# Optimization experiments

Hardware: AMD Instinct MI355X
Metric: run time of the kernel (lower is better)

The kernel has to match this reference:

```python
import jax, jax.numpy as jnp
import numpy as np

S, B, D, H = 2048, 2, 2048, 16
HD = D // H  # 128
EPS = 1e-5


def _layernorm(x, w, b):
    mu = jnp.mean(x, axis=-1, keepdims=True)
    var = jnp.mean((x - mu) ** 2, axis=-1, keepdims=True)
    return (x - mu) * jax.lax.rsqrt(var + EPS) * w + b


def _apply_rotary(x, freqs_cis):
    # x: [B, S, H, HD]; freqs_cis: [S, HD//2, 2]
    xr = x.astype(jnp.float32).reshape(x.shape[0], x.shape[1], x.shape[2], HD // 2, 2)
    f = freqs_cis.reshape(1, xr.shape[1], 1, xr.shape[3], 2)
    out = jnp.stack(
        [xr[..., 0] * f[..., 0] - xr[..., 1] * f[..., 1],
         xr[..., 1] * f[..., 0] + xr[..., 0] * f[..., 1]],
        axis=-1,
    )
    return out.reshape(x.shape).astype(x.dtype)


def setup_inputs() -> dict:
    key = jax.random.key(0)
    ks = jax.random.split(key, 6)
    scale = 0.02
    return {
        "x": jax.random.normal(ks[0], (S, B, D), dtype=jnp.float32),
        "freqs_cis": jax.random.normal(ks[1], (S, HD // 2, 2), dtype=jnp.float32),
        "wqkv_w": jax.random.normal(ks[2], (3 * D, D), dtype=jnp.float32) * scale,
        "wqkv_b": jnp.zeros((3 * D,), dtype=jnp.float32),
        "wo_w": jax.random.normal(ks[3], (D, D), dtype=jnp.float32) * scale,
        "wo_b": jnp.zeros((D,), dtype=jnp.float32),
        "qn_w": jnp.ones((HD,), dtype=jnp.float32),
        "qn_b": jnp.zeros((HD,), dtype=jnp.float32),
        "kn_w": jnp.ones((HD,), dtype=jnp.float32),
        "kn_b": jnp.zeros((HD,), dtype=jnp.float32),
    }


def reference(x, freqs_cis, wqkv_w, wqkv_b, wo_w, wo_b, qn_w, qn_b, kn_w, kn_b):
    # x: [S, B, D] -> [B, S, D]
    xb = jnp.transpose(x, (1, 0, 2))
    qkv = jnp.einsum("bsd,ed->bse", xb, wqkv_w) + wqkv_b  # [B, S, 3D]
    xq, xk, xv = jnp.split(qkv, 3, axis=-1)
    xq = xq.reshape(B, S, H, HD)
    xk = xk.reshape(B, S, H, HD)
    xv = xv.reshape(B, S, H, HD)
    # QK-norm over head_dim
    xq = _layernorm(xq, qn_w, qn_b)
    xk = _layernorm(xk, kn_w, kn_b)
    # RoPE
    xq = _apply_rotary(xq, freqs_cis)
    xk = _apply_rotary(xk, freqs_cis)
    # [B, H, S, HD]
    q = jnp.transpose(xq, (0, 2, 1, 3))
    k = jnp.transpose(xk, (0, 2, 1, 3))
    v = jnp.transpose(xv, (0, 2, 1, 3))
    scores = jnp.einsum("bhqd,bhkd->bhqk", q, k) / jnp.sqrt(jnp.float32(HD))
    causal = jnp.tril(jnp.ones((S, S), dtype=bool))
    scores = jnp.where(causal, scores, jnp.finfo(scores.dtype).min)
    attn = jax.nn.softmax(scores, axis=-1)
    out = jnp.einsum("bhqk,bhkd->bhqd", attn, v)  # [B, H, S, HD]
    out = jnp.transpose(out, (0, 2, 1, 3)).reshape(B, S, D)
    out = jnp.einsum("bsd,ed->bse", out, wo_w) + wo_b
    return jnp.transpose(out, (1, 0, 2))  # [S, B, D]
```

## Files before the change

### kernel.cpp

```cpp
#include <hip/hip_runtime.h>
#include <hip/hip_bf16.h>

#define S 2048
#define B 2
#define D 2048
#define H 16
#define HD 128
#define N3 6144
#define KD 2048

typedef __hip_bfloat16 bf16;
typedef float f32x4 __attribute__((ext_vector_type(4)));
typedef short short8 __attribute__((ext_vector_type(8)));
typedef short sv4 __attribute__((ext_vector_type(4)));

__device__ __forceinline__ void gload16(const void* g, void* l) {
    __builtin_amdgcn_global_load_lds((const __attribute__((address_space(1))) void*)g,
                                     (__attribute__((address_space(3))) void*)l, 16, 0, 0);
}
__device__ __forceinline__ void bar() {
    asm volatile("" ::: "memory");
    __builtin_amdgcn_s_barrier();
    asm volatile("" ::: "memory");
}

__global__ __launch_bounds__(256) void cvt_x_kernel(const float* __restrict__ x, bf16* __restrict__ xb) {
    int i = blockIdx.x * 256 + threadIdx.x;
    int d  = i & (D - 1);
    int sb = i >> 11;
    int b  = sb & (B - 1);
    int s  = sb >> 1;
    xb[((size_t)(b * S + s) << 11) + d] = __float2bfloat16(x[i]);
}

__global__ __launch_bounds__(256) void cvt_w_kernel(const float* __restrict__ in, bf16* __restrict__ o, int n) {
    for (int i = blockIdx.x * blockDim.x + threadIdx.x; i < n; i += gridDim.x * blockDim.x)
        o[i] = __float2bfloat16(in[i]);
}

template <int MODE>
__global__ __launch_bounds__(256, 2) void gemm128(
    const bf16* __restrict__ A, const bf16* __restrict__ W, const float* __restrict__ bias,
    bf16* __restrict__ oq, bf16* __restrict__ ok, bf16* __restrict__ ovT,
    float* __restrict__ oOut)
{
    constexpr int NT = KD / 64;

    __shared__ __align__(16) bf16 SA[2][128 * 64];
    __shared__ __align__(16) bf16 SB[2][128 * 64];

    const int tid = threadIdx.x;
    const int w = tid >> 6, l = tid & 63;
    const int wm = w >> 1, wn = w & 1;
    const int l15 = l & 15, l4 = l >> 4;

    const int id  = blockIdx.y * gridDim.x + blockIdx.x;
    const int xcd = id & 7;
    const int j   = id >> 3;
    const int npx = gridDim.x >> 3;
    const int tileN = (xcd * npx + j % npx) * 128;
    const int tileM = (j / npx) * 128;

    const int lrow8 = l >> 3;
    const int lsb   = ((l & 7) * 16) ^ (lrow8 << 4);
    const int rxor  = (l15 & 7) << 3;

    const char* AgT = (const char*)A + (size_t)tileM * (KD * 2);
    const char* WgT = (const char*)W + (size_t)tileN * (KD * 2);

    auto stage_tile = [&](int buf, int kt) {
#pragma unroll
        for (int j2 = 0; j2 < 4; ++j2) {
            const int chunk = w * 4 + j2;
            gload16(AgT + (size_t)(chunk * 8 + lrow8) * (KD * 2) + kt * 128 + lsb,
                    (char*)&SA[buf][0] + chunk * 1024);
        }
#pragma unroll
        for (int j2 = 0; j2 < 4; ++j2) {
            const int chunk = w * 4 + j2;
            gload16(WgT + (size_t)(chunk * 8 + lrow8) * (KD * 2) + kt * 128 + lsb,
                    (char*)&SB[buf][0] + chunk * 1024);
        }
    };

    f32x4 acc[4][4] = {};

#define TILE_BODY(BUF, KTN)                                                                \
    {                                                                                      \
        stage_tile(BUF ^ 1, KTN);                                                          \
        _Pragma("unroll") for (int kk = 0; kk < 2; ++kk) {                                 \
            short8 bfrag[4], afr[4];                                                       \
            _Pragma("unroll") for (int ni = 0; ni < 4; ++ni)                               \
                bfrag[ni] = *(const short8*)&SB[BUF][(wn * 64 + ni * 16 + l15) * 64 +      \
                                                     ((kk * 32 + l4 * 8) ^ rxor)];         \
            _Pragma("unroll") for (int q = 0; q < 4; ++q)                                  \
                afr[q] = *(const short8*)&SA[BUF][(wm * 64 + q * 16 + l15) * 64 +          \
                                                  ((kk * 32 + l4 * 8) ^ rxor)];            \
            __builtin_amdgcn_s_setprio(1);                                                 \
            _Pragma("unroll") for (int q = 0; q < 4; ++q)                                  \
                _Pragma("unroll") for (int ni = 0; ni < 4; ++ni)                           \
                    acc[q][ni] = __builtin_amdgcn_mfma_f32_16x16x32_bf16(                  \
                        afr[q], bfrag[ni], acc[q][ni], 0, 0, 0);                           \
            __builtin_amdgcn_s_setprio(0);                                                 \
        }                                                                                  \
        asm volatile("s_waitcnt vmcnt(0)" ::: "memory");                                   \
        bar();                                                                             \
    }

    stage_tile(0, 0);
    asm volatile("s_waitcnt vmcnt(0)" ::: "memory");
    bar();

#pragma unroll 1
    for (int t = 0; t < NT; t += 2) {
        const int tn1 = (t + 1 < NT) ? t + 1 : NT - 1;
        const int tn2 = (t + 2 < NT) ? t + 2 : NT - 1;
        TILE_BODY(0, tn1)
        TILE_BODY(1, tn2)
    }
#undef TILE_BODY

#pragma unroll
    for (int mi = 0; mi < 4; ++mi) {
#pragma unroll
        for (int ni = 0; ni < 4; ++ni) {
            const int ncol = tileN + wn * 64 + ni * 16 + l15;
            const float bv = bias[ncol];
            const int m0 = tileM + wm * 64 + mi * 16 + l4 * 4;
            if (MODE == 0) {
                const int b_ = m0 >> 11, s0 = m0 & (S - 1);
                const int which = ncol >> 11;
                const int hh = (ncol >> 7) & (H - 1);
                const int hd = ncol & (HD - 1);
                const int bh = b_ * H + hh;
                if (which == 2) {
                    sv4 pk;
#pragma unroll
                    for (int r = 0; r < 4; ++r) {
                        __hip_bfloat16 t = __float2bfloat16(acc[mi][ni][r] + bv);
                        pk[r] = reinterpret_cast<short&>(t);
                    }
                    *(sv4*)&ovT[((size_t)bh * HD + hd) * S + s0] = pk;
                } else {
                    bf16* dst = which ? ok : oq;
#pragma unroll
                    for (int r = 0; r < 4; ++r)
                        dst[((size_t)bh * S + s0 + r) * HD + hd] =
                            __float2bfloat16(acc[mi][ni][r] + bv);
                }
            } else {
#pragma unroll
                for (int r = 0; r < 4; ++r) {
                    const int m = m0 + r;
                    const int b_ = m >> 11, s_ = m & (S - 1);
                    oOut[((size_t)s_ * B + b_) * D + ncol] = acc[mi][ni][r] + bv;
                }
            }
        }
    }
}

__global__ __launch_bounds__(256) void ln_rope_kernel(
    bf16* __restrict__ q, bf16* __restrict__ k,
    const float* __restrict__ fc,
    const float* __restrict__ qw, const float* __restrict__ qb,
    const float* __restrict__ kw, const float* __restrict__ kb)
{
    const int tid = threadIdx.x;
    const int w = tid >> 6, l = tid & 63;
    const int row = blockIdx.x * 4 + w;
    const int s_ = row & (S - 1);
    const size_t base = (size_t)row * HD;
    const float f0 = fc[s_ * HD + 2 * l];
    const float f1 = fc[s_ * HD + 2 * l + 1];

#pragma unroll
    for (int which = 0; which < 2; ++which) {
        bf16* p = which == 0 ? q : k;
        const float* gw = which == 0 ? qw : kw;
        const float* gb = which == 0 ? qb : kb;
        const float osc = which == 0 ? 0.08838834764831845f : 1.0f;
        float x0 = __bfloat162float(p[base + 2 * l]);
        float x1 = __bfloat162float(p[base + 2 * l + 1]);
        float sm = x0 + x1;
#pragma unroll
        for (int msk = 1; msk < 64; msk <<= 1) sm += __shfl_xor(sm, msk);
        const float mu = sm * (1.0f / HD);
        const float d0 = x0 - mu, d1 = x1 - mu;
        float vs = d0 * d0 + d1 * d1;
#pragma unroll
        for (int msk = 1; msk < 64; msk <<= 1) vs += __shfl_xor(vs, msk);
        const float rstd = rsqrtf(vs * (1.0f / HD) + 1e-5f);
        const float n0 = d0 * rstd * gw[2 * l] + gb[2 * l];
        const float n1 = d1 * rstd * gw[2 * l + 1] + gb[2 * l + 1];
        p[base + 2 * l]     = __float2bfloat16((n0 * f0 - n1 * f1) * osc);
        p[base + 2 * l + 1] = __float2bfloat16((n1 * f0 + n0 * f1) * osc);
    }
}

__global__ __launch_bounds__(256, 2) void attn_kernel(
    const bf16* __restrict__ q, const bf16* __restrict__ k, const bf16* __restrict__ vT,
    bf16* __restrict__ out)
{
    __shared__ __align__(16) bf16 KT[2][64 * 128];
    __shared__ __align__(16) bf16 VS[2][128 * 64];
    __shared__ __align__(16) bf16 Pb[4][16 * 72];

    const int tid = threadIdx.x, w = tid >> 6, l = tid & 63;
    const int l15 = l & 15, l4 = l >> 4;

    const int id  = blockIdx.y * gridDim.x + blockIdx.x;
    const int nid = (id & 7) * 64 + (id >> 3);
    const int bh  = nid >> 4;
    const int pr  = nid & 15;
    const int qtA = 31 - pr;
    const int qtB = pr;

    const int b_ = bh >> 4, hh = bh & (H - 1);
    const int qrA = qtA * 64 + w * 16;
    const int qrB = qtB * 64 + w * 16;
    const size_t hQ = (size_t)bh * S * HD;
    const size_t hV = (size_t)bh * HD * S;

    const char* kbase = (const char*)(k + hQ);
    const char* vbase = (const char*)(vT + hV);
    int ksrc[4], vsrc[4], kdst[4], vdst[4];
#pragma unroll
    for (int j = 0; j < 4; ++j) {
        const int ik = w * 4 + j;
        const int rt = ik * 4 + (l >> 4);
        ksrc[j] = rt * 256 + (((l & 15) * 16) ^ ((rt & 15) << 4));
        kdst[j] = ik * 1024;
        const int rd = ik * 8 + (l >> 3);
        vsrc[j] = rd * (S * 2) + (((l & 7) * 16) ^ ((rd & 7) << 4));
        vdst[j] = ik * 1024;
    }

    short8 aqA[4], aqB[4];
#pragma unroll
    for (int c = 0; c < 4; ++c) {
        aqA[c] = *(const short8*)&q[hQ + (size_t)(qrA + l15) * HD + c * 32 + l4 * 8];
        aqB[c] = *(const short8*)&q[hQ + (size_t)(qrB + l15) * HD + c * 32 + l4 * 8];
    }

    f32x4 oA[8] = {}, oB[8] = {};
    float psA[4] = {0.f, 0.f, 0.f, 0.f}, psB[4] = {0.f, 0.f, 0.f, 0.f};

#pragma unroll
    for (int j = 0; j < 4; ++j)
        gload16(kbase + ksrc[j], (char*)KT[0] + kdst[j]);

    const int kx = l15 << 3;
    const int vx = (l15 & 7) << 3;
    const float LOG2E = 1.4426950408889634f;
    const float SHIFT = -23.083120654223414f;

    for (int kvt = 0; kvt <= qtA; ++kvt) {
        const int kvb = kvt * 64;
        const int cur = kvt & 1;
        const bool doB = (kvt <= qtB);
#pragma unroll
        for (int j = 0; j < 4; ++j)
            gload16(vbase + (size_t)kvb * 2 + vsrc[j], (char*)VS[cur] + vdst[j]);
        if (kvt < qtA) {
#pragma unroll
            for (int j = 0; j < 4; ++j)
                gload16(kbase + (size_t)(kvb + 64) * 256 + ksrc[j], (char*)KT[cur ^ 1] + kdst[j]);
        }
        if (kvt < qtA) { asm volatile("s_waitcnt vmcnt(8)" ::: "memory"); }
        else           { asm volatile("s_waitcnt vmcnt(4)" ::: "memory"); }
        bar();

        short8 apA[2], apB[2];
        {
            f32x4 sacc[4] = {};
#pragma unroll
            for (int c = 0; c < 4; ++c) {
                const int cole = (c * 32 + l4 * 8) ^ kx;
#pragma unroll
                for (int n = 0; n < 4; ++n) {
                    short8 bk = *(const short8*)&KT[cur][(n * 16 + l15) * 128 + cole];
                    sacc[n] = __builtin_amdgcn_mfma_f32_16x16x32_bf16(aqA[c], bk, sacc[n], 0, 0, 0);
                }
            }
            if (kvt == qtA) {
#pragma unroll
                for (int n = 0; n < 4; ++n)
#pragma unroll
                    for (int r = 0; r < 4; ++r) {
                        float sv = (kvb + n * 16 + l15 > qrA + l4 * 4 + r) ? -1e30f : sacc[n][r];
                        const float pv = __builtin_amdgcn_exp2f(__builtin_fmaf(sv, LOG2E, SHIFT));
                        sacc[n][r] = pv; psA[r] += pv;
                    }
            } else {
#pragma unroll
                for (int n = 0; n < 4; ++n)
#pragma unroll
                    for (int r = 0; r < 4; ++r) {
                        const float pv = __builtin_amdgcn_exp2f(__builtin_fmaf(sacc[n][r], LOG2E, SHIFT));
                        sacc[n][r] = pv; psA[r] += pv;
                    }
            }
#pragma unroll
            for (int n = 0; n < 4; ++n)
#pragma unroll
                for (int r = 0; r < 4; ++r)
                    Pb[w][(l4 * 4 + r) * 72 + n * 16 + l15] = __float2bfloat16(sacc[n][r]);
#pragma unroll
            for (int c = 0; c < 2; ++c)
                apA[c] = *(const short8*)&Pb[w][l15 * 72 + c * 32 + l4 * 8];
        }
        if (doB) {
            f32x4 sacc[4] = {};
#pragma unroll
            for (int c = 0; c < 4; ++c) {
                const int cole = (c * 32 + l4 * 8) ^ kx;
#pragma unroll
                for (int n = 0; n < 4; ++n) {
                    short8 bk = *(const short8*)&KT[cur][(n * 16 + l15) * 128 + cole];
                    sacc[n] = __builtin_amdgcn_mfma_f32_16x16x32_bf16(aqB[c], bk, sacc[n], 0, 0, 0);
                }
            }
            if (kvt == qtB) {
#pragma unroll
                for (int n = 0; n < 4; ++n)
#pragma unroll
                    for (int r = 0; r < 4; ++r) {
                        float sv = (kvb + n * 16 + l15 > qrB + l4 * 4 + r) ? -1e30f : sacc[n][r];
                        const float pv = __builtin_amdgcn_exp2f(__builtin_fmaf(sv, LOG2E, SHIFT));
                        sacc[n][r] = pv; psB[r] += pv;
                    }
            } else {
#pragma unroll
                for (int n = 0; n < 4; ++n)
#pragma unroll
                    for (int r = 0; r < 4; ++r) {
                        const float pv = __builtin_amdgcn_exp2f(__builtin_fmaf(sacc[n][r], LOG2E, SHIFT));
                        sacc[n][r] = pv; psB[r] += pv;
                    }
            }
#pragma unroll
            for (int n = 0; n < 4; ++n)
#pragma unroll
                for (int r = 0; r < 4; ++r)
                    Pb[w][(l4 * 4 + r) * 72 + n * 16 + l15] = __float2bfloat16(sacc[n][r]);
#pragma unroll
            for (int c = 0; c < 2; ++c)
                apB[c] = *(const short8*)&Pb[w][l15 * 72 + c * 32 + l4 * 8];
        }

        if (kvt < qtA) { asm volatile("s_waitcnt vmcnt(4)" ::: "memory"); }
        else           { asm volatile("s_waitcnt vmcnt(0)" ::: "memory"); }
        bar();

#pragma unroll
        for (int c = 0; c < 2; ++c) {
#pragma unroll
            for (int d = 0; d < 8; ++d) {
                const int rd = d * 16 + l15;
                short8 bv = *(const short8*)&VS[cur][rd * 64 + ((c * 32 + l4 * 8) ^ vx)];
                oA[d] = __builtin_amdgcn_mfma_f32_16x16x32_bf16(apA[c], bv, oA[d], 0, 0, 0);
            }
        }
        if (doB) {
#pragma unroll
            for (int c = 0; c < 2; ++c) {
#pragma unroll
                for (int d = 0; d < 8; ++d) {
                    const int rd = d * 16 + l15;
                    short8 bv = *(const short8*)&VS[cur][rd * 64 + ((c * 32 + l4 * 8) ^ vx)];
                    oB[d] = __builtin_amdgcn_mfma_f32_16x16x32_bf16(apB[c], bv, oB[d], 0, 0, 0);
                }
            }
        }
    }

#pragma unroll
    for (int r = 0; r < 4; ++r) {
#pragma unroll
        for (int msk = 1; msk < 16; msk <<= 1) psA[r] += __shfl_xor(psA[r], msk);
        const float inv = 1.0f / psA[r];
        const int s_ = qrA + l4 * 4 + r;
        const size_t obase = ((size_t)b_ * S + s_) * D + hh * HD;
#pragma unroll
        for (int d = 0; d < 8; ++d)
            out[obase + d * 16 + l15] = __float2bfloat16(oA[d][r] * inv);
    }
#pragma unroll
    for (int r = 0; r < 4; ++r) {
#pragma unroll
        for (int msk = 1; msk < 16; msk <<= 1) psB[r] += __shfl_xor(psB[r], msk);
        const float inv = 1.0f / psB[r];
        const int s_ = qrB + l4 * 4 + r;
        const size_t obase = ((size_t)b_ * S + s_) * D + hh * HD;
#pragma unroll
        for (int d = 0; d < 8; ++d)
            out[obase + d * 16 + l15] = __float2bfloat16(oB[d][r] * inv);
    }
}

extern "C" void kernel_launch(void* const* d_in, const int* in_sizes, int n_in,
                              void* d_out, int out_size, void* d_ws, size_t ws_size,
                              hipStream_t stream) {
    const float* x      = (const float*)d_in[0];
    const float* fc     = (const float*)d_in[1];
    const float* wqkv_w = (const float*)d_in[2];
    const float* wqkv_b = (const float*)d_in[3];
    const float* wo_w   = (const float*)d_in[4];
    const float* wo_b   = (const float*)d_in[5];
    const float* qn_w   = (const float*)d_in[6];
    const float* qn_b   = (const float*)d_in[7];
    const float* kn_w   = (const float*)d_in[8];
    const float* kn_b   = (const float*)d_in[9];
    float* out = (float*)d_out;
    char* ws = (char*)d_ws;

    bf16* xb = (bf16*)(ws);
    bf16* w1 = (bf16*)(ws + 16777216);
    bf16* wo = (bf16*)(ws + 41943040);
    bf16* qb = (bf16*)(ws + 50331648);
    bf16* kb = (bf16*)(ws + 67108864);
    bf16* vT = (bf16*)(ws + 83886080);
    bf16* ao = (bf16*)(ws + 100663296);

    cvt_x_kernel<<<(S * B * D) / 256, 256, 0, stream>>>(x, xb);
    cvt_w_kernel<<<4096, 256, 0, stream>>>(wqkv_w, w1, N3 * D);
    cvt_w_kernel<<<2048, 256, 0, stream>>>(wo_w, wo, D * D);

    gemm128<0><<<dim3(N3 / 128, (B * S) / 128), 256, 0, stream>>>(
        xb, w1, wqkv_b, qb, kb, vT, nullptr);

    ln_rope_kernel<<<(B * H * S) / 4, 256, 0, stream>>>(qb, kb, fc, qn_w, qn_b, kn_w, kn_b);

    attn_kernel<<<dim3(16, B * H), 256, 0, stream>>>(qb, kb, vT, ao);

    gemm128<1><<<dim3(D / 128, (B * S) / 128), 256, 0, stream>>>(
        ao, wo, wo_b, nullptr, nullptr, nullptr, out);
}
```

Measured before the change: 259.3 us.

## Fuse QK layernorm and RoPE into QKV GEMM epilogue; interleave attention A/B tiles

```diff
diff --git a/kernel.cpp b/kernel.cpp
--- a/kernel.cpp
+++ b/kernel.cpp
@@ -42,7 +42,10 @@
 __global__ __launch_bounds__(256, 2) void gemm128(
     const bf16* __restrict__ A, const bf16* __restrict__ W, const float* __restrict__ bias,
     bf16* __restrict__ oq, bf16* __restrict__ ok, bf16* __restrict__ ovT,
-    float* __restrict__ oOut)
+    float* __restrict__ oOut,
+    const float* __restrict__ fc,
+    const float* __restrict__ qn_w, const float* __restrict__ qn_b,
+    const float* __restrict__ kn_w, const float* __restrict__ kn_b)
 {
     constexpr int NT = KD / 64;
 
@@ -120,35 +123,14 @@
     }
 #undef TILE_BODY
 
-#pragma unroll
-    for (int mi = 0; mi < 4; ++mi) {
-#pragma unroll
-        for (int ni = 0; ni < 4; ++ni) {
-            const int ncol = tileN + wn * 64 + ni * 16 + l15;
-            const float bv = bias[ncol];
-            const int m0 = tileM + wm * 64 + mi * 16 + l4 * 4;
-            if (MODE == 0) {
-                const int b_ = m0 >> 11, s0 = m0 & (S - 1);
-                const int which = ncol >> 11;
-                const int hh = (ncol >> 7) & (H - 1);
-                const int hd = ncol & (HD - 1);
-                const int bh = b_ * H + hh;
-                if (which == 2) {
-                    sv4 pk;
-#pragma unroll
-                    for (int r = 0; r < 4; ++r) {
-                        __hip_bfloat16 t = __float2bfloat16(acc[mi][ni][r] + bv);
-                        pk[r] = reinterpret_cast<short&>(t);
-                    }
-                    *(sv4*)&ovT[((size_t)bh * HD + hd) * S + s0] = pk;
-                } else {
-                    bf16* dst = which ? ok : oq;
-#pragma unroll
-                    for (int r = 0; r < 4; ++r)
-                        dst[((size_t)bh * S + s0 + r) * HD + hd] =
-                            __float2bfloat16(acc[mi][ni][r] + bv);
-                }
-            } else {
+    if (MODE == 1) {
+#pragma unroll
+        for (int mi = 0; mi < 4; ++mi) {
+#pragma unroll
+            for (int ni = 0; ni < 4; ++ni) {
+                const int ncol = tileN + wn * 64 + ni * 16 + l15;
+                const float bv = bias[ncol];
+                const int m0 = tileM + wm * 64 + mi * 16 + l4 * 4;
 #pragma unroll
                 for (int r = 0; r < 4; ++r) {
                     const int m = m0 + r;
@@ -157,44 +139,104 @@
                 }
             }
         }
-    }
-}
-
-__global__ __launch_bounds__(256) void ln_rope_kernel(
-    bf16* __restrict__ q, bf16* __restrict__ k,
-    const float* __restrict__ fc,
-    const float* __restrict__ qw, const float* __restrict__ qb,
-    const float* __restrict__ kw, const float* __restrict__ kb)
-{
-    const int tid = threadIdx.x;
-    const int w = tid >> 6, l = tid & 63;
-    const int row = blockIdx.x * 4 + w;
-    const int s_ = row & (S - 1);
-    const size_t base = (size_t)row * HD;
-    const float f0 = fc[s_ * HD + 2 * l];
-    const float f1 = fc[s_ * HD + 2 * l + 1];
-
-#pragma unroll
-    for (int which = 0; which < 2; ++which) {
-        bf16* p = which == 0 ? q : k;
-        const float* gw = which == 0 ? qw : kw;
-        const float* gb = which == 0 ? qb : kb;
-        const float osc = which == 0 ? 0.08838834764831845f : 1.0f;
-        float x0 = __bfloat162float(p[base + 2 * l]);
-        float x1 = __bfloat162float(p[base + 2 * l + 1]);
-        float sm = x0 + x1;
-#pragma unroll
-        for (int msk = 1; msk < 64; msk <<= 1) sm += __shfl_xor(sm, msk);
-        const float mu = sm * (1.0f / HD);
-        const float d0 = x0 - mu, d1 = x1 - mu;
-        float vs = d0 * d0 + d1 * d1;
-#pragma unroll
-        for (int msk = 1; msk < 64; msk <<= 1) vs += __shfl_xor(vs, msk);
-        const float rstd = rsqrtf(vs * (1.0f / HD) + 1e-5f);
-        const float n0 = d0 * rstd * gw[2 * l] + gb[2 * l];
-        const float n1 = d1 * rstd * gw[2 * l + 1] + gb[2 * l + 1];
-        p[base + 2 * l]     = __float2bfloat16((n0 * f0 - n1 * f1) * osc);
-        p[base + 2 * l + 1] = __float2bfloat16((n1 * f0 + n0 * f1) * osc);
+        return;
+    }
+
+    const int which = tileN >> 11;
+    const int hh = (tileN >> 7) & (H - 1);
+
+    if (which == 2) {
+#pragma unroll
+        for (int mi = 0; mi < 4; ++mi) {
+#pragma unroll
+            for (int ni = 0; ni < 4; ++ni) {
+                const int ncol = tileN + wn * 64 + ni * 16 + l15;
+                const float bv = bias[ncol];
+                const int m0 = tileM + wm * 64 + mi * 16 + l4 * 4;
+                const int b_ = m0 >> 11, s0 = m0 & (S - 1);
+                const int hd = ncol & (HD - 1);
+                const int bh = b_ * H + hh;
+                sv4 pk;
+#pragma unroll
+                for (int r = 0; r < 4; ++r) {
+                    __hip_bfloat16 t = __float2bfloat16(acc[mi][ni][r] + bv);
+                    pk[r] = reinterpret_cast<short&>(t);
+                }
+                *(sv4*)&ovT[((size_t)bh * HD + hd) * S + s0] = pk;
+            }
+        }
+        return;
+    }
+
+    {
+        float* fbuf = (float*)&SA[0][0];
+        const float* gw  = which ? kn_w : qn_w;
+        const float* gb  = which ? kn_b : qn_b;
+        const float osc  = which ? 1.0f : 0.08838834764831845f;
+        bf16* dst = which ? ok : oq;
+
+        const int colh = wn * 64 + l15;
+        float bvs[4];
+#pragma unroll
+        for (int ni = 0; ni < 4; ++ni) bvs[ni] = bias[tileN + colh + ni * 16];
+#pragma unroll
+        for (int mi = 0; mi < 4; ++mi)
+#pragma unroll
+            for (int ni = 0; ni < 4; ++ni)
+#pragma unroll
+                for (int r = 0; r < 4; ++r) acc[mi][ni][r] += bvs[ni];
+
+#pragma unroll
+        for (int mi = 0; mi < 4; ++mi) {
+#pragma unroll
+            for (int r = 0; r < 4; ++r) {
+                float s1 = 0.f, s2 = 0.f;
+#pragma unroll
+                for (int ni = 0; ni < 4; ++ni) {
+                    const float v = acc[mi][ni][r];
+                    s1 += v; s2 += v * v;
+                }
+#pragma unroll
+                for (int msk = 1; msk < 16; msk <<= 1) {
+                    s1 += __shfl_xor(s1, msk);
+                    s2 += __shfl_xor(s2, msk);
+                }
+                const int rloc = wm * 64 + mi * 16 + l4 * 4 + r;
+                if (l15 == 0) {
+                    fbuf[wn * 128 + rloc] = s1;
+                    fbuf[256 + wn * 128 + rloc] = s2;
+                }
+            }
+        }
+        bar();
+
+#pragma unroll
+        for (int mi = 0; mi < 4; ++mi) {
+#pragma unroll
+            for (int r = 0; r < 4; ++r) {
+                const int rloc = wm * 64 + mi * 16 + l4 * 4 + r;
+                const float tot1 = fbuf[rloc] + fbuf[128 + rloc];
+                const float tot2 = fbuf[256 + rloc] + fbuf[384 + rloc];
+                const float mu = tot1 * (1.0f / HD);
+                const float var = tot2 * (1.0f / HD) - mu * mu;
+                const float rstd = rsqrtf(var + 1e-5f);
+                const int m = tileM + wm * 64 + mi * 16 + l4 * 4 + r;
+                const int b_ = m >> 11, s_ = m & (S - 1);
+                const size_t obase = ((size_t)(b_ * H + hh) * S + s_) * (size_t)HD;
+                const float* fcr = fc + (size_t)s_ * HD;
+#pragma unroll
+                for (int ni = 0; ni < 4; ++ni) {
+                    const int col = colh + ni * 16;
+                    const float nv = (acc[mi][ni][r] - mu) * rstd * gw[col] + gb[col];
+                    const float pv = __shfl_xor(nv, 1);
+                    const int cp = col & ~1;
+                    const float f0 = fcr[cp], f1 = fcr[cp + 1];
+                    const float rot = (l15 & 1) ? (nv * f0 + pv * f1)
+                                                : (nv * f0 - pv * f1);
+                    dst[obase + col] = __float2bfloat16(rot * osc);
+                }
+            }
+        }
     }
 }
 
@@ -271,79 +313,71 @@
         else           { asm volatile("s_waitcnt vmcnt(4)" ::: "memory"); }
         bar();
 
+        f32x4 sA[4] = {}, sB[4] = {};
+#pragma unroll
+        for (int c = 0; c < 4; ++c) {
+            const int cole = (c * 32 + l4 * 8) ^ kx;
+#pragma unroll
+            for (int n = 0; n < 4; ++n) {
+                short8 bk = *(const short8*)&KT[cur][(n * 16 + l15) * 128 + cole];
+                sA[n] = __builtin_amdgcn_mfma_f32_16x16x32_bf16(aqA[c], bk, sA[n], 0, 0, 0);
+                if (doB)
+                    sB[n] = __builtin_amdgcn_mfma_f32_16x16x32_bf16(aqB[c], bk, sB[n], 0, 0, 0);
+            }
+        }
+
         short8 apA[2], apB[2];
-        {
-            f32x4 sacc[4] = {};
-#pragma unroll
-            for (int c = 0; c < 4; ++c) {
-                const int cole = (c * 32 + l4 * 8) ^ kx;
-#pragma unroll
-                for (int n = 0; n < 4; ++n) {
-                    short8 bk = *(const short8*)&KT[cur][(n * 16 + l15) * 128 + cole];
-                    sacc[n] = __builtin_amdgcn_mfma_f32_16x16x32_bf16(aqA[c], bk, sacc[n], 0, 0, 0);
-                }
-            }
-            if (kvt == qtA) {
+        if (kvt == qtA) {
+#pragma unroll
+            for (int n = 0; n < 4; ++n)
+#pragma unroll
+                for (int r = 0; r < 4; ++r) {
+                    float sv = (kvb + n * 16 + l15 > qrA + l4 * 4 + r) ? -1e30f : sA[n][r];
+                    const float pv = __builtin_amdgcn_exp2f(__builtin_fmaf(sv, LOG2E, SHIFT));
+                    sA[n][r] = pv; psA[r] += pv;
+                }
+        } else {
+#pragma unroll
+            for (int n = 0; n < 4; ++n)
+#pragma unroll
+                for (int r = 0; r < 4; ++r) {
+                    const float pv = __builtin_amdgcn_exp2f(__builtin_fmaf(sA[n][r], LOG2E, SHIFT));
+                    sA[n][r] = pv; psA[r] += pv;
+                }
+        }
+#pragma unroll
+        for (int n = 0; n < 4; ++n)
+#pragma unroll
+            for (int r = 0; r < 4; ++r)
+                Pb[w][(l4 * 4 + r) * 72 + n * 16 + l15] = __float2bfloat16(sA[n][r]);
+#pragma unroll
+        for (int c = 0; c < 2; ++c)
+            apA[c] = *(const short8*)&Pb[w][l15 * 72 + c * 32 + l4 * 8];
+
+        if (doB) {
+            if (kvt == qtB) {
 #pragma unroll
                 for (int n = 0; n < 4; ++n)
 #pragma unroll
                     for (int r = 0; r < 4; ++r) {
-                        float sv = (kvb + n * 16 + l15 > qrA + l4 * 4 + r) ? -1e30f : sacc[n][r];
+                        float sv = (kvb + n * 16 + l15 > qrB + l4 * 4 + r) ? -1e30f : sB[n][r];
                         const float pv = __builtin_amdgcn_exp2f(__builtin_fmaf(sv, LOG2E, SHIFT));
-                        sacc[n][r] = pv; psA[r] += pv;
+                        sB[n][r] = pv; psB[r] += pv;
                     }
             } else {
 #pragma unroll
                 for (int n = 0; n < 4; ++n)
 #pragma unroll
                     for (int r = 0; r < 4; ++r) {
-                        const float pv = __builtin_amdgcn_exp2f(__builtin_fmaf(sacc[n][r], LOG2E, SHIFT));
-                        sacc[n][r] = pv; psA[r] += pv;
+                        const float pv = __builtin_amdgcn_exp2f(__builtin_fmaf(sB[n][r], LOG2E, SHIFT));
+                        sB[n][r] = pv; psB[r] += pv;
                     }
             }
 #pragma unroll
             for (int n = 0; n < 4; ++n)
 #pragma unroll
                 for (int r = 0; r < 4; ++r)
-                    Pb[w][(l4 * 4 + r) * 72 + n * 16 + l15] = __float2bfloat16(sacc[n][r]);
-#pragma unroll
-            for (int c = 0; c < 2; ++c)
-                apA[c] = *(const short8*)&Pb[w][l15 * 72 + c * 32 + l4 * 8];
-        }
-        if (doB) {
-            f32x4 sacc[4] = {};
-#pragma unroll
-            for (int c = 0; c < 4; ++c) {
-                const int cole = (c * 32 + l4 * 8) ^ kx;
-#pragma unroll
-                for (int n = 0; n < 4; ++n) {
-                    short8 bk = *(const short8*)&KT[cur][(n * 16 + l15) * 128 + cole];
-                    sacc[n] = __builtin_amdgcn_mfma_f32_16x16x32_bf16(aqB[c], bk, sacc[n], 0, 0, 0);
-                }
-            }
-            if (kvt == qtB) {
-#pragma unroll
-                for (int n = 0; n < 4; ++n)
-#pragma unroll
-                    for (int r = 0; r < 4; ++r) {
-                        float sv = (kvb + n * 16 + l15 > qrB + l4 * 4 + r) ? -1e30f : sacc[n][r];
-                        const float pv = __builtin_amdgcn_exp2f(__builtin_fmaf(sv, LOG2E, SHIFT));
-                        sacc[n][r] = pv; psB[r] += pv;
-                    }
-            } else {
-#pragma unroll
-                for (int n = 0; n < 4; ++n)
-#pragma unroll
-                    for (int r = 0; r < 4; ++r) {
-                        const float pv = __builtin_amdgcn_exp2f(__builtin_fmaf(sacc[n][r], LOG2E, SHIFT));
-                        sacc[n][r] = pv; psB[r] += pv;
-                    }
-            }
-#pragma unroll
-            for (int n = 0; n < 4; ++n)
-#pragma unroll
-                for (int r = 0; r < 4; ++r)
-                    Pb[w][(l4 * 4 + r) * 72 + n * 16 + l15] = __float2bfloat16(sacc[n][r]);
+                    Pb[w][(l4 * 4 + r) * 72 + n * 16 + l15] = __float2bfloat16(sB[n][r]);
 #pragma unroll
             for (int c = 0; c < 2; ++c)
                 apB[c] = *(const short8*)&Pb[w][l15 * 72 + c * 32 + l4 * 8];
@@ -360,17 +394,8 @@
                 const int rd = d * 16 + l15;
                 short8 bv = *(const short8*)&VS[cur][rd * 64 + ((c * 32 + l4 * 8) ^ vx)];
                 oA[d] = __builtin_amdgcn_mfma_f32_16x16x32_bf16(apA[c], bv, oA[d], 0, 0, 0);
-            }
-        }
-        if (doB) {
-#pragma unroll
-            for (int c = 0; c < 2; ++c) {
-#pragma unroll
-                for (int d = 0; d < 8; ++d) {
-                    const int rd = d * 16 + l15;
-                    short8 bv = *(const short8*)&VS[cur][rd * 64 + ((c * 32 + l4 * 8) ^ vx)];
+                if (doB)
                     oB[d] = __builtin_amdgcn_mfma_f32_16x16x32_bf16(apB[c], bv, oB[d], 0, 0, 0);
-                }
             }
         }
     }
@@ -428,12 +453,12 @@
     cvt_w_kernel<<<2048, 256, 0, stream>>>(wo_w, wo, D * D);
 
     gemm128<0><<<dim3(N3 / 128, (B * S) / 128), 256, 0, stream>>>(
-        xb, w1, wqkv_b, qb, kb, vT, nullptr);
-
-    ln_rope_kernel<<<(B * H * S) / 4, 256, 0, stream>>>(qb, kb, fc, qn_w, qn_b, kn_w, kn_b);
+        xb, w1, wqkv_b, qb, kb, vT, nullptr,
+        fc, qn_w, qn_b, kn_w, kn_b);
 
     attn_kernel<<<dim3(16, B * H), 256, 0, stream>>>(qb, kb, vT, ao);
 
     gemm128<1><<<dim3(D / 128, (B * S) / 128), 256, 0, stream>>>(
-        ao, wo, wo_b, nullptr, nullptr, nullptr, out);
-}
+        ao, wo, wo_b, nullptr, nullptr, nullptr, out,
+        nullptr, nullptr, nullptr, nullptr, nullptr);
+}
```

After: 274.0 us. 5.7% more time.

## Vectorize fp32-to-bf16 conversions and share K/V LDS reads across attention query tiles

Applied to the files above, without the earlier changes.

```diff
diff --git a/kernel.cpp b/kernel.cpp
--- a/kernel.cpp
+++ b/kernel.cpp
@@ -24,18 +24,32 @@
     asm volatile("" ::: "memory");
 }
 
+__device__ __forceinline__ short8 cvt8(const float* p) {
+    f32x4 a = *(const f32x4*)p;
+    f32x4 b = *(const f32x4*)(p + 4);
+    short8 r;
+#pragma unroll
+    for (int j = 0; j < 4; ++j) {
+        __hip_bfloat16 t0 = __float2bfloat16(a[j]);
+        __hip_bfloat16 t1 = __float2bfloat16(b[j]);
+        r[j]     = reinterpret_cast<short&>(t0);
+        r[j + 4] = reinterpret_cast<short&>(t1);
+    }
+    return r;
+}
+
 __global__ __launch_bounds__(256) void cvt_x_kernel(const float* __restrict__ x, bf16* __restrict__ xb) {
-    int i = blockIdx.x * 256 + threadIdx.x;
+    int i = (blockIdx.x * 256 + threadIdx.x) * 8;
     int d  = i & (D - 1);
     int sb = i >> 11;
     int b  = sb & (B - 1);
     int s  = sb >> 1;
-    xb[((size_t)(b * S + s) << 11) + d] = __float2bfloat16(x[i]);
+    *(short8*)&xb[((size_t)(b * S + s) << 11) + d] = cvt8(x + i);
 }
 
 __global__ __launch_bounds__(256) void cvt_w_kernel(const float* __restrict__ in, bf16* __restrict__ o, int n) {
-    for (int i = blockIdx.x * blockDim.x + threadIdx.x; i < n; i += gridDim.x * blockDim.x)
-        o[i] = __float2bfloat16(in[i]);
+    for (int i = (blockIdx.x * blockDim.x + threadIdx.x) * 8; i < n; i += gridDim.x * blockDim.x * 8)
+        *(short8*)&o[i] = cvt8(in + i);
 }
 
 template <int MODE>
@@ -271,79 +285,71 @@
         else           { asm volatile("s_waitcnt vmcnt(4)" ::: "memory"); }
         bar();
 
+        f32x4 sA[4] = {}, sB[4] = {};
+#pragma unroll
+        for (int c = 0; c < 4; ++c) {
+            const int cole = (c * 32 + l4 * 8) ^ kx;
+#pragma unroll
+            for (int n = 0; n < 4; ++n) {
+                short8 bk = *(const short8*)&KT[cur][(n * 16 + l15) * 128 + cole];
+                sA[n] = __builtin_amdgcn_mfma_f32_16x16x32_bf16(aqA[c], bk, sA[n], 0, 0, 0);
+                if (doB)
+                    sB[n] = __builtin_amdgcn_mfma_f32_16x16x32_bf16(aqB[c], bk, sB[n], 0, 0, 0);
+            }
+        }
+
         short8 apA[2], apB[2];
-        {
-            f32x4 sacc[4] = {};
-#pragma unroll
-            for (int c = 0; c < 4; ++c) {
-                const int cole = (c * 32 + l4 * 8) ^ kx;
-#pragma unroll
-                for (int n = 0; n < 4; ++n) {
-                    short8 bk = *(const short8*)&KT[cur][(n * 16 + l15) * 128 + cole];
-                    sacc[n] = __builtin_amdgcn_mfma_f32_16x16x32_bf16(aqA[c], bk, sacc[n], 0, 0, 0);
+        if (kvt == qtA) {
+#pragma unroll
+            for (int n = 0; n < 4; ++n)
+#pragma unroll
+                for (int r = 0; r < 4; ++r) {
+                    float sv = (kvb + n * 16 + l15 > qrA + l4 * 4 + r) ? -1e30f : sA[n][r];
+                    const float pv = __builtin_amdgcn_exp2f(__builtin_fmaf(sv, LOG2E, SHIFT));
+                    sA[n][r] = pv; psA[r] += pv;
                 }
-            }
-            if (kvt == qtA) {
+        } else {
+#pragma unroll
+            for (int n = 0; n < 4; ++n)
+#pragma unroll
+                for (int r = 0; r < 4; ++r) {
+                    const float pv = __builtin_amdgcn_exp2f(__builtin_fmaf(sA[n][r], LOG2E, SHIFT));
+                    sA[n][r] = pv; psA[r] += pv;
+                }
+        }
+#pragma unroll
+        for (int n = 0; n < 4; ++n)
+#pragma unroll
+            for (int r = 0; r < 4; ++r)
+                Pb[w][(l4 * 4 + r) * 72 + n * 16 + l15] = __float2bfloat16(sA[n][r]);
+#pragma unroll
+        for (int c = 0; c < 2; ++c)
+            apA[c] = *(const short8*)&Pb[w][l15 * 72 + c * 32 + l4 * 8];
+
+        if (doB) {
+            if (kvt == qtB) {
 #pragma unroll
                 for (int n = 0; n < 4; ++n)
 #pragma unroll
                     for (int r = 0; r < 4; ++r) {
-                        float sv = (kvb + n * 16 + l15 > qrA + l4 * 4 + r) ? -1e30f : sacc[n][r];
+                        float sv = (kvb + n * 16 + l15 > qrB + l4 * 4 + r) ? -1e30f : sB[n][r];
                         const float pv = __builtin_amdgcn_exp2f(__builtin_fmaf(sv, LOG2E, SHIFT));
-                        sacc[n][r] = pv; psA[r] += pv;
+                        sB[n][r] = pv; psB[r] += pv;
                     }
             } else {
 #pragma unroll
                 for (int n = 0; n < 4; ++n)
 #pragma unroll
                     for (int r = 0; r < 4; ++r) {
-                        const float pv = __builtin_amdgcn_exp2f(__builtin_fmaf(sacc[n][r], LOG2E, SHIFT));
-                        sacc[n][r] = pv; psA[r] += pv;
+                        const float pv = __builtin_amdgcn_exp2f(__builtin_fmaf(sB[n][r], LOG2E, SHIFT));
+                        sB[n][r] = pv; psB[r] += pv;
                     }
             }
 #pragma unroll
             for (int n = 0; n < 4; ++n)
 #pragma unroll
                 for (int r = 0; r < 4; ++r)
-                    Pb[w][(l4 * 4 + r) * 72 + n * 16 + l15] = __float2bfloat16(sacc[n][r]);
-#pragma unroll
-            for (int c = 0; c < 2; ++c)
-                apA[c] = *(const short8*)&Pb[w][l15 * 72 + c * 32 + l4 * 8];
-        }
-        if (doB) {
-            f32x4 sacc[4] = {};
-#pragma unroll
-            for (int c = 0; c < 4; ++c) {
-                const int cole = (c * 32 + l4 * 8) ^ kx;
-#pragma unroll
-                for (int n = 0; n < 4; ++n) {
-                    short8 bk = *(const short8*)&KT[cur][(n * 16 + l15) * 128 + cole];
-                    sacc[n] = __builtin_amdgcn_mfma_f32_16x16x32_bf16(aqB[c], bk, sacc[n], 0, 0, 0);
-                }
-            }
-            if (kvt == qtB) {
-#pragma unroll
-                for (int n = 0; n < 4; ++n)
-#pragma unroll
-                    for (int r = 0; r < 4; ++r) {
-                        float sv = (kvb + n * 16 + l15 > qrB + l4 * 4 + r) ? -1e30f : sacc[n][r];
-                        const float pv = __builtin_amdgcn_exp2f(__builtin_fmaf(sv, LOG2E, SHIFT));
-                        sacc[n][r] = pv; psB[r] += pv;
-                    }
-            } else {
-#pragma unroll
-                for (int n = 0; n < 4; ++n)
-#pragma unroll
-                    for (int r = 0; r < 4; ++r) {
-                        const float pv = __builtin_amdgcn_exp2f(__builtin_fmaf(sacc[n][r], LOG2E, SHIFT));
-                        sacc[n][r] = pv; psB[r] += pv;
-                    }
-            }
-#pragma unroll
-            for (int n = 0; n < 4; ++n)
-#pragma unroll
-                for (int r = 0; r < 4; ++r)
-                    Pb[w][(l4 * 4 + r) * 72 + n * 16 + l15] = __float2bfloat16(sacc[n][r]);
+                    Pb[w][(l4 * 4 + r) * 72 + n * 16 + l15] = __float2bfloat16(sB[n][r]);
 #pragma unroll
             for (int c = 0; c < 2; ++c)
                 apB[c] = *(const short8*)&Pb[w][l15 * 72 + c * 32 + l4 * 8];
@@ -360,17 +366,8 @@
                 const int rd = d * 16 + l15;
                 short8 bv = *(const short8*)&VS[cur][rd * 64 + ((c * 32 + l4 * 8) ^ vx)];
                 oA[d] = __builtin_amdgcn_mfma_f32_16x16x32_bf16(apA[c], bv, oA[d], 0, 0, 0);
-            }
-        }
-        if (doB) {
-#pragma unroll
-            for (int c = 0; c < 2; ++c) {
-#pragma unroll
-                for (int d = 0; d < 8; ++d) {
-                    const int rd = d * 16 + l15;
-                    short8 bv = *(const short8*)&VS[cur][rd * 64 + ((c * 32 + l4 * 8) ^ vx)];
+                if (doB)
                     oB[d] = __builtin_amdgcn_mfma_f32_16x16x32_bf16(apB[c], bv, oB[d], 0, 0, 0);
-                }
             }
         }
     }
@@ -423,9 +420,9 @@
     bf16* vT = (bf16*)(ws + 83886080);
     bf16* ao = (bf16*)(ws + 100663296);
 
-    cvt_x_kernel<<<(S * B * D) / 256, 256, 0, stream>>>(x, xb);
-    cvt_w_kernel<<<4096, 256, 0, stream>>>(wqkv_w, w1, N3 * D);
-    cvt_w_kernel<<<2048, 256, 0, stream>>>(wo_w, wo, D * D);
+    cvt_x_kernel<<<(S * B * D) / (256 * 8), 256, 0, stream>>>(x, xb);
+    cvt_w_kernel<<<2048, 256, 0, stream>>>(wqkv_w, w1, N3 * D);
+    cvt_w_kernel<<<1024, 256, 0, stream>>>(wo_w, wo, D * D);
 
     gemm128<0><<<dim3(N3 / 128, (B * S) / 128), 256, 0, stream>>>(
         xb, w1, wqkv_b, qb, kb, vT, nullptr);
```

Result: slower. 272.2 us (+5.0%).
